# Performance work log

Hardware: AMD Instinct MI355X
Metric: run time of the kernel (lower is better)

The kernel has to match this reference:

```python
import jax, jax.numpy as jnp
import numpy as np

N_T, N_I = 4096, 4096
TEXT_DIM, IMAGE_DIM, HIDDEN_DIM = 1024, 1024, 1024


def setup_inputs() -> dict:
    key = jax.random.key(0)
    ks = jax.random.split(key, 8)
    s_t = 1.0 / np.sqrt(TEXT_DIM)
    s_i = 1.0 / np.sqrt(IMAGE_DIM)
    return {
        "text_features": jax.random.normal(ks[0], (N_T, TEXT_DIM), jnp.float32),
        "image_features": jax.random.normal(ks[1], (N_I, IMAGE_DIM), jnp.float32),
        # nn.Linear params: weight [out, in], bias [out]
        "w_text": jax.random.uniform(ks[2], (HIDDEN_DIM, TEXT_DIM), jnp.float32, -s_t, s_t),
        "b_text": jax.random.uniform(ks[3], (HIDDEN_DIM,), jnp.float32, -s_t, s_t),
        "w_image": jax.random.uniform(ks[4], (HIDDEN_DIM, IMAGE_DIM), jnp.float32, -s_i, s_i),
        "b_image": jax.random.uniform(ks[5], (HIDDEN_DIM,), jnp.float32, -s_i, s_i),
        "scale_TI": jnp.ones((1,), jnp.float32),
        "scale_IT": jnp.ones((1,), jnp.float32),
    }


def reference(text_features, image_features, w_text, b_text, w_image, b_image, scale_TI, scale_IT):
    # linear projections to shared hidden space
    t = text_features @ w_text.T + b_text      # [N_t, H]
    i = image_features @ w_image.T + b_image   # [N_i, H]
    inv_sqrt_h = 1.0 / jnp.sqrt(jnp.asarray(HIDDEN_DIM, t.dtype))
    # text -> image attention: softmax over image axis, scaled post-softmax
    logits_TI = (t @ i.T) * inv_sqrt_h               # [N_t, N_i]
    attn_TI = jax.nn.softmax(logits_TI, axis=-1) * scale_TI
    # image -> text attention
    attn_IT = jax.nn.softmax(logits_TI.T, axis=-1) * scale_IT  # [N_i, N_t]
    text_attention_on_image = attn_TI @ image_features  # [N_t, image_dim]
    image_attention_on_text = attn_IT @ text_features   # [N_i, text_dim]
    return (text_attention_on_image, image_attention_on_text)
```

## Files before the change

### kernel.cpp

```cpp
#include <hip/hip_runtime.h>


typedef __bf16 bf16x8 __attribute__((ext_vector_type(8)));
typedef float f32x4 __attribute__((ext_vector_type(4)));

#define N_T 4096
#define N_I 4096
#define DIM 1024
#define TSS 136

__device__ __forceinline__ unsigned short f2bf(float f) {
    unsigned int u = __float_as_uint(f);
    u += 0x7fffu + ((u >> 16) & 1u);
    return (unsigned short)(u >> 16);
}

__device__ __forceinline__ void async_cp16(const unsigned short* g, unsigned short* l) {
    __builtin_amdgcn_global_load_lds(
        (const __attribute__((address_space(1))) unsigned int*)g,
        (__attribute__((address_space(3))) unsigned int*)l, 16, 0, 0);
}

__device__ __forceinline__ void stage_async(const unsigned short* __restrict__ src,
                                            int ld, int row0, int k0,
                                            unsigned short* lds, int t) {
    int r = t >> 2, c = (t & 3) << 3;
    const unsigned short* g = src + (size_t)(row0 + r) * ld + k0 + c;
    async_cp16(g, lds + r * 32 + c);
    async_cp16(g + (size_t)64 * ld, lds + (64 + r) * 32 + c);
}

__device__ __forceinline__ void mfma_step(const unsigned short* As,
                                          const unsigned short* Bs, f32x4 acc[4][4],
                                          int wrow, int wcol, int lane16, int quad) {
    bf16x8 a[4], b[4];
#pragma unroll
    for (int i = 0; i < 4; ++i) {
        a[i] = *(const bf16x8*)&As[(wrow + i * 16 + lane16) * 32 + quad * 8];
        b[i] = *(const bf16x8*)&Bs[(wcol + i * 16 + lane16) * 32 + quad * 8];
    }
#pragma unroll
    for (int i = 0; i < 4; ++i)
#pragma unroll
        for (int j = 0; j < 4; ++j)
            acc[i][j] = __builtin_amdgcn_mfma_f32_16x16x32_bf16(a[i], b[j], acc[i][j], 0, 0, 0);
}

__device__ __forceinline__ void tile_store(const unsigned short* sm,
                                           unsigned short* __restrict__ g, int ld,
                                           int row0, int col0, int tid) {
    int r = tid >> 1, h = (tid & 1) << 6;
    const unsigned short* src = sm + r * TSS + h;
    unsigned short* dst = g + (size_t)(row0 + r) * ld + col0 + h;
#pragma unroll
    for (int v = 0; v < 8; ++v)
        *(uint4*)(dst + v * 8) = *(const uint4*)(src + v * 8);
}

__global__ void __launch_bounds__(256)
cvt_all(const float* __restrict__ im, const float* __restrict__ tx,
        const float* __restrict__ wt, const float* __restrict__ wi,
        unsigned short* __restrict__ imb, unsigned short* __restrict__ txb,
        unsigned short* __restrict__ imgT, unsigned short* __restrict__ textT,
        unsigned short* __restrict__ wtb, unsigned short* __restrict__ wib,
        float* __restrict__ lTI) {
    int t = threadIdx.x;
    if (blockIdx.z == 2) {
        int lin = blockIdx.y * 64 + blockIdx.x;
        if (lin < 4) {
            *(f32x4*)&lTI[(lin * 256 + t) * 8] = (f32x4){0.f, 0.f, 0.f, 0.f};
            *(f32x4*)&lTI[(lin * 256 + t) * 8 + 4] = (f32x4){0.f, 0.f, 0.f, 0.f};
        }
        size_t i = (size_t)(lin * 256 + t) * 8;
        const float* s;
        unsigned short* d;
        size_t off;
        if (i < 1048576) { s = wt; d = wtb; off = i; }
        else             { s = wi; d = wib; off = i - 1048576; }
        float4 f0 = *(const float4*)(s + off);
        float4 f1 = *(const float4*)(s + off + 4);
        uint4 o;
        o.x = (unsigned int)f2bf(f0.x) | ((unsigned int)f2bf(f0.y) << 16);
        o.y = (unsigned int)f2bf(f0.z) | ((unsigned int)f2bf(f0.w) << 16);
        o.z = (unsigned int)f2bf(f1.x) | ((unsigned int)f2bf(f1.y) << 16);
        o.w = (unsigned int)f2bf(f1.z) | ((unsigned int)f2bf(f1.w) << 16);
        *(uint4*)(d + off) = o;
        return;
    }
    const float* in = blockIdx.z ? tx : im;
    unsigned short* nb = blockIdx.z ? txb : imb;
    unsigned short* tr = blockIdx.z ? textT : imgT;
    __shared__ float tile[64][65];
    int row0 = blockIdx.x * 64, col0 = blockIdx.y * 64;
    int r = t >> 2, c = (t & 3) << 4;
    {
        const float* p = in + (size_t)(row0 + r) * DIM + col0 + c;
        float4 f0 = *(const float4*)(p);
        float4 f1 = *(const float4*)(p + 4);
        float4 f2 = *(const float4*)(p + 8);
        float4 f3 = *(const float4*)(p + 12);
        *(float4*)&tile[r][c] = f0;
        *(float4*)&tile[r][c + 4] = f1;
        *(float4*)&tile[r][c + 8] = f2;
        *(float4*)&tile[r][c + 12] = f3;
        uint4 o0, o1;
        o0.x = (unsigned int)f2bf(f0.x) | ((unsigned int)f2bf(f0.y) << 16);
        o0.y = (unsigned int)f2bf(f0.z) | ((unsigned int)f2bf(f0.w) << 16);
        o0.z = (unsigned int)f2bf(f1.x) | ((unsigned int)f2bf(f1.y) << 16);
        o0.w = (unsigned int)f2bf(f1.z) | ((unsigned int)f2bf(f1.w) << 16);
        o1.x = (unsigned int)f2bf(f2.x) | ((unsigned int)f2bf(f2.y) << 16);
        o1.y = (unsigned int)f2bf(f2.z) | ((unsigned int)f2bf(f2.w) << 16);
        o1.z = (unsigned int)f2bf(f3.x) | ((unsigned int)f2bf(f3.y) << 16);
        o1.w = (unsigned int)f2bf(f3.z) | ((unsigned int)f2bf(f3.w) << 16);
        unsigned short* q = nb + (size_t)(row0 + r) * DIM + col0 + c;
        *(uint4*)q = o0;
        *(uint4*)(q + 8) = o1;
    }
    __syncthreads();
    {
        int cr = r, cc = c;
        unsigned short v[16];
#pragma unroll
        for (int u = 0; u < 16; ++u) v[u] = f2bf(tile[cc + u][cr]);
        unsigned short* q = tr + (size_t)(col0 + cr) * N_T + row0 + cc;
        *(uint4*)q = *(uint4*)&v[0];
        *(uint4*)(q + 8) = *(uint4*)&v[8];
    }
}

__global__ void __launch_bounds__(256, 4)
gemm_proj2(const unsigned short* __restrict__ Atx, const unsigned short* __restrict__ Wtx,
           const float* __restrict__ btx, unsigned short* __restrict__ Ctx,
           const unsigned short* __restrict__ Aim, const unsigned short* __restrict__ Wim,
           const float* __restrict__ bim, unsigned short* __restrict__ Cim) {
    __shared__ unsigned short As[2][128 * 32];
    __shared__ unsigned short Bs[2][128 * 32];
    int z = blockIdx.z;
    const unsigned short* A = z ? Aim : Atx;
    const unsigned short* W = z ? Wim : Wtx;
    const float* bias = z ? bim : btx;
    unsigned short* C = z ? Cim : Ctx;
    int tid = threadIdx.x;
    int m0 = blockIdx.x * 128, n0 = blockIdx.y * 128;
    int lane = tid & 63, wave = tid >> 6;
    int lane16 = lane & 15, quad = lane >> 4;
    int wrow = (wave >> 1) * 64, wcol = (wave & 1) * 64;
    f32x4 acc[4][4];
    {
        f32x4 zz = {0.f, 0.f, 0.f, 0.f};
        for (int i = 0; i < 4; ++i)
            for (int j = 0; j < 4; ++j) acc[i][j] = zz;
    }
    for (int k0 = 0; k0 < DIM; k0 += 64) {
        stage_async(A, DIM, m0, k0, As[0], tid);
        stage_async(W, DIM, n0, k0, Bs[0], tid);
        stage_async(A, DIM, m0, k0 + 32, As[1], tid);
        stage_async(W, DIM, n0, k0 + 32, Bs[1], tid);
        __syncthreads();
        mfma_step(As[0], Bs[0], acc, wrow, wcol, lane16, quad);
        mfma_step(As[1], Bs[1], acc, wrow, wcol, lane16, quad);
        __syncthreads();
    }
#pragma unroll
    for (int j = 0; j < 4; ++j) {
        int col = n0 + wcol + j * 16 + lane16;
        float bv = bias[col];
#pragma unroll
        for (int i = 0; i < 4; ++i) {
            int rowb = m0 + wrow + i * 16 + quad * 4;
#pragma unroll
            for (int r = 0; r < 4; ++r)
                C[(size_t)(rowb + r) * DIM + col] = f2bf(acc[i][j][r] + bv);
        }
    }
}

__global__ void __launch_bounds__(256, 4)
gemm_logits_exp(const unsigned short* __restrict__ Tb,
                const unsigned short* __restrict__ Ib,
                unsigned short* __restrict__ P, unsigned short* __restrict__ PT,
                float* __restrict__ lT, float* __restrict__ lI) {
    __shared__ unsigned short smem[128 * TSS];
    unsigned short* As0 = smem;
    unsigned short* Bs0 = smem + 4096;
    unsigned short* As1 = smem + 8192;
    unsigned short* Bs1 = smem + 12288;
    int tid = threadIdx.x;
    int m0 = blockIdx.x * 128, n0 = blockIdx.y * 128;
    int lane = tid & 63, wave = tid >> 6;
    int lane16 = lane & 15, quad = lane >> 4;
    int wrow = (wave >> 1) * 64, wcol = (wave & 1) * 64;
    f32x4 acc[4][4];
    {
        f32x4 z = {0.f, 0.f, 0.f, 0.f};
        for (int i = 0; i < 4; ++i)
            for (int j = 0; j < 4; ++j) acc[i][j] = z;
    }
    for (int k0 = 0; k0 < DIM; k0 += 64) {
        stage_async(Tb, DIM, m0, k0, As0, tid);
        stage_async(Ib, DIM, n0, k0, Bs0, tid);
        stage_async(Tb, DIM, m0, k0 + 32, As1, tid);
        stage_async(Ib, DIM, n0, k0 + 32, Bs1, tid);
        __syncthreads();
        mfma_step(As0, Bs0, acc, wrow, wcol, lane16, quad);
        mfma_step(As1, Bs1, acc, wrow, wcol, lane16, quad);
        __syncthreads();
    }
#pragma unroll
    for (int i = 0; i < 4; ++i)
#pragma unroll
        for (int j = 0; j < 4; ++j)
#pragma unroll
            for (int r = 0; r < 4; ++r)
                acc[i][j][r] = __expf(acc[i][j][r] * 0.03125f);
#pragma unroll
    for (int i = 0; i < 4; ++i)
#pragma unroll
        for (int r = 0; r < 4; ++r) {
            float s = acc[i][0][r] + acc[i][1][r] + acc[i][2][r] + acc[i][3][r];
            s += __shfl_xor(s, 1); s += __shfl_xor(s, 2);
            s += __shfl_xor(s, 4); s += __shfl_xor(s, 8);
            if (lane16 == 0) atomicAdd(&lT[m0 + wrow + i * 16 + quad * 4 + r], s);
        }
#pragma unroll
    for (int j = 0; j < 4; ++j) {
        float s = 0.f;
#pragma unroll
        for (int i = 0; i < 4; ++i)
#pragma unroll
            for (int r = 0; r < 4; ++r) s += acc[i][j][r];
        s += __shfl_xor(s, 16); s += __shfl_xor(s, 32);
        if (quad == 0) atomicAdd(&lI[n0 + wcol + j * 16 + lane16], s);
    }
    __syncthreads();
#pragma unroll
    for (int i = 0; i < 4; ++i)
#pragma unroll
        for (int j = 0; j < 4; ++j)
#pragma unroll
            for (int r = 0; r < 4; ++r)
                smem[(wrow + i * 16 + quad * 4 + r) * TSS + wcol + j * 16 + lane16] =
                    f2bf(acc[i][j][r]);
    __syncthreads();
    tile_store(smem, P, N_I, m0, n0, tid);
    __syncthreads();
#pragma unroll
    for (int i = 0; i < 4; ++i)
#pragma unroll
        for (int j = 0; j < 4; ++j) {
            unsigned int lo = (unsigned int)f2bf(acc[i][j][0]) |
                              ((unsigned int)f2bf(acc[i][j][1]) << 16);
            unsigned int hi = (unsigned int)f2bf(acc[i][j][2]) |
                              ((unsigned int)f2bf(acc[i][j][3]) << 16);
            uint2 v; v.x = lo; v.y = hi;
            *(uint2*)&smem[(wcol + j * 16 + lane16) * TSS + wrow + i * 16 + quad * 4] = v;
        }
    __syncthreads();
    tile_store(smem, PT, N_T, n0, m0, tid);
}

__global__ void __launch_bounds__(512, 4)
gemm_attn2(const unsigned short* __restrict__ P, const unsigned short* __restrict__ imgT,
           const float* __restrict__ lT, const float* __restrict__ sTI,
           float* __restrict__ out0,
           const unsigned short* __restrict__ PT, const unsigned short* __restrict__ textT,
           const float* __restrict__ lI, const float* __restrict__ sIT,
           float* __restrict__ out1) {
    __shared__ unsigned short As[2][2][128 * 32];
    __shared__ unsigned short Bs[2][2][128 * 32];
    int which = blockIdx.z;
    const unsigned short* A = which ? PT : P;
    const unsigned short* Bt = which ? textT : imgT;
    const float* l = which ? lI : lT;
    const float* sp = which ? sIT : sTI;
    float* out = which ? out1 : out0;

    int tid = threadIdx.x;
    int half = tid >> 8;
    int t = tid & 255;
    int m0 = blockIdx.x * 128, n0 = blockIdx.y * 128;
    int lane = tid & 63;
    int wv = (tid >> 6) & 3;
    int lane16 = lane & 15, quad = lane >> 4;
    int wrow = (wv >> 1) * 64, wcol = (wv & 1) * 64;
    f32x4 acc[4][4];
    {
        f32x4 z = {0.f, 0.f, 0.f, 0.f};
        for (int i = 0; i < 4; ++i)
            for (int j = 0; j < 4; ++j) acc[i][j] = z;
    }

    int kbeg = half * 2048;
    for (int k0 = kbeg; k0 < kbeg + 2048; k0 += 64) {
        stage_async(A, 4096, m0, k0, As[half][0], t);
        stage_async(Bt, 4096, n0, k0, Bs[half][0], t);
        stage_async(A, 4096, m0, k0 + 32, As[half][1], t);
        stage_async(Bt, 4096, n0, k0 + 32, Bs[half][1], t);
        __syncthreads();
        mfma_step(As[half][0], Bs[half][0], acc, wrow, wcol, lane16, quad);
        mfma_step(As[half][1], Bs[half][1], acc, wrow, wcol, lane16, quad);
        __syncthreads();
    }

    float* red = (float*)As;
#pragma unroll
    for (int i = 0; i < 4; ++i) {
        __syncthreads();
        if (half) {
#pragma unroll
            for (int j = 0; j < 4; ++j)
                *(f32x4*)&red[wv * 1024 + lane * 16 + j * 4] = acc[i][j];
        }
        __syncthreads();
        if (!half) {
#pragma unroll
            for (int j = 0; j < 4; ++j)
                acc[i][j] += *(const f32x4*)&red[wv * 1024 + lane * 16 + j * 4];
        }
    }
    if (half) return;

    float sc = sp[0];
#pragma unroll
    for (int i = 0; i < 4; ++i) {
        int rowb = m0 + wrow + i * 16 + quad * 4;
        float fac[4];
#pragma unroll
        for (int r = 0; r < 4; ++r) fac[r] = sc / l[rowb + r];
#pragma unroll
        for (int j = 0; j < 4; ++j) {
            int col = n0 + wcol + j * 16 + lane16;
#pragma unroll
            for (int r = 0; r < 4; ++r)
                out[(size_t)(rowb + r) * DIM + col] = acc[i][j][r] * fac[r];
        }
    }
}

extern "C" void kernel_launch(void* const* d_in, const int* in_sizes, int n_in,
                              void* d_out, int out_size, void* d_ws, size_t ws_size,
                              hipStream_t stream) {
    const float* text = (const float*)d_in[0];
    const float* image = (const float*)d_in[1];
    const float* w_text = (const float*)d_in[2];
    const float* b_text = (const float*)d_in[3];
    const float* w_image = (const float*)d_in[4];
    const float* b_image = (const float*)d_in[5];
    const float* scale_TI = (const float*)d_in[6];
    const float* scale_IT = (const float*)d_in[7];
    float* out0 = (float*)d_out;
    float* out1 = out0 + (size_t)N_T * DIM;

    char* ws = (char*)d_ws;
    unsigned short* text_bf = (unsigned short*)(ws);
    unsigned short* image_bf = (unsigned short*)(ws + (8ull << 20));
    unsigned short* wt_bf = (unsigned short*)(ws + (16ull << 20));
    unsigned short* wi_bf = (unsigned short*)(ws + (18ull << 20));
    unsigned short* P = (unsigned short*)(ws);
    unsigned short* imgT = (unsigned short*)(ws + (32ull << 20));
    unsigned short* textT = (unsigned short*)(ws + (40ull << 20));
    unsigned short* t_bf = (unsigned short*)(ws + (48ull << 20));
    unsigned short* i_bf = (unsigned short*)(ws + (56ull << 20));
    unsigned short* PT = (unsigned short*)(ws + (64ull << 20));
    float* lT = (float*)(ws + (96ull << 20));
    float* lI = (float*)(ws + (96ull << 20) + 16384);

    cvt_all<<<dim3(N_T / 64, DIM / 64, 3), 256, 0, stream>>>(
        image, text, w_text, w_image, image_bf, text_bf, imgT, textT,
        wt_bf, wi_bf, lT);

    gemm_proj2<<<dim3(N_T / 128, DIM / 128, 2), 256, 0, stream>>>(
        text_bf, wt_bf, b_text, t_bf, image_bf, wi_bf, b_image, i_bf);

    gemm_logits_exp<<<dim3(N_T / 128, N_I / 128), 256, 0, stream>>>(t_bf, i_bf, P, PT, lT, lI);

    gemm_attn2<<<dim3(N_T / 128, DIM / 128, 2), 512, 0, stream>>>(
        P, imgT, lT, scale_TI, out0, PT, textT, lI, scale_IT, out1);
}
```

Measured before the change: 267.1 us.

## Halve proj tile width, pre-reduce softmax sums in LDS, split attn epilogue

The projection GEMM now uses 128x64 tiles, doubling the grid to 1024 blocks so the GPU's compute units are better filled. In the logits kernel, row and column exp-sums are first combined across wave pairs in shared memory, which halves the global atomicAdds. In the split-K attention kernel, the reduction now runs in two steps with fewer barriers, and both halves share the scaling and output stores. The cost is less data reuse per block in the projection GEMM and a small amount of extra LDS and synchronisation in the logits kernel.

```diff
diff --git a/kernel.cpp b/kernel.cpp
--- a/kernel.cpp
+++ b/kernel.cpp
@@ -30,6 +30,13 @@
     async_cp16(g + (size_t)64 * ld, lds + (64 + r) * 32 + c);
 }
 
+__device__ __forceinline__ void stage_async64(const unsigned short* __restrict__ src,
+                                              int ld, int row0, int k0,
+                                              unsigned short* lds, int t) {
+    int r = t >> 2, c = (t & 3) << 3;
+    async_cp16(src + (size_t)(row0 + r) * ld + k0 + c, lds + r * 32 + c);
+}
+
 __device__ __forceinline__ void mfma_step(const unsigned short* As,
                                           const unsigned short* Bs, f32x4 acc[4][4],
                                           int wrow, int wcol, int lane16, int quad) {
@@ -43,6 +50,23 @@
     for (int i = 0; i < 4; ++i)
 #pragma unroll
         for (int j = 0; j < 4; ++j)
+            acc[i][j] = __builtin_amdgcn_mfma_f32_16x16x32_bf16(a[i], b[j], acc[i][j], 0, 0, 0);
+}
+
+__device__ __forceinline__ void mfma_step42(const unsigned short* As,
+                                            const unsigned short* Bs, f32x4 acc[4][2],
+                                            int wrow, int wcol, int lane16, int quad) {
+    bf16x8 a[4], b[2];
+#pragma unroll
+    for (int i = 0; i < 4; ++i)
+        a[i] = *(const bf16x8*)&As[(wrow + i * 16 + lane16) * 32 + quad * 8];
+#pragma unroll
+    for (int j = 0; j < 2; ++j)
+        b[j] = *(const bf16x8*)&Bs[(wcol + j * 16 + lane16) * 32 + quad * 8];
+#pragma unroll
+    for (int i = 0; i < 4; ++i)
+#pragma unroll
+        for (int j = 0; j < 2; ++j)
             acc[i][j] = __builtin_amdgcn_mfma_f32_16x16x32_bf16(a[i], b[j], acc[i][j], 0, 0, 0);
 }
 
@@ -118,11 +142,10 @@
     }
     __syncthreads();
     {
-        int cr = r, cc = c;
         unsigned short v[16];
 #pragma unroll
-        for (int u = 0; u < 16; ++u) v[u] = f2bf(tile[cc + u][cr]);
-        unsigned short* q = tr + (size_t)(col0 + cr) * N_T + row0 + cc;
+        for (int u = 0; u < 16; ++u) v[u] = f2bf(tile[c + u][r]);
+        unsigned short* q = tr + (size_t)(col0 + r) * N_T + row0 + c;
         *(uint4*)q = *(uint4*)&v[0];
         *(uint4*)(q + 8) = *(uint4*)&v[8];
     }
@@ -134,35 +157,35 @@
            const unsigned short* __restrict__ Aim, const unsigned short* __restrict__ Wim,
            const float* __restrict__ bim, unsigned short* __restrict__ Cim) {
     __shared__ unsigned short As[2][128 * 32];
-    __shared__ unsigned short Bs[2][128 * 32];
+    __shared__ unsigned short Bs[2][64 * 32];
     int z = blockIdx.z;
     const unsigned short* A = z ? Aim : Atx;
     const unsigned short* W = z ? Wim : Wtx;
     const float* bias = z ? bim : btx;
     unsigned short* C = z ? Cim : Ctx;
     int tid = threadIdx.x;
-    int m0 = blockIdx.x * 128, n0 = blockIdx.y * 128;
+    int m0 = blockIdx.x * 128, n0 = blockIdx.y * 64;
     int lane = tid & 63, wave = tid >> 6;
     int lane16 = lane & 15, quad = lane >> 4;
-    int wrow = (wave >> 1) * 64, wcol = (wave & 1) * 64;
-    f32x4 acc[4][4];
+    int wrow = (wave >> 1) * 64, wcol = (wave & 1) * 32;
+    f32x4 acc[4][2];
     {
         f32x4 zz = {0.f, 0.f, 0.f, 0.f};
         for (int i = 0; i < 4; ++i)
-            for (int j = 0; j < 4; ++j) acc[i][j] = zz;
+            for (int j = 0; j < 2; ++j) acc[i][j] = zz;
     }
     for (int k0 = 0; k0 < DIM; k0 += 64) {
         stage_async(A, DIM, m0, k0, As[0], tid);
-        stage_async(W, DIM, n0, k0, Bs[0], tid);
+        stage_async64(W, DIM, n0, k0, Bs[0], tid);
         stage_async(A, DIM, m0, k0 + 32, As[1], tid);
-        stage_async(W, DIM, n0, k0 + 32, Bs[1], tid);
-        __syncthreads();
-        mfma_step(As[0], Bs[0], acc, wrow, wcol, lane16, quad);
-        mfma_step(As[1], Bs[1], acc, wrow, wcol, lane16, quad);
-        __syncthreads();
-    }
-#pragma unroll
-    for (int j = 0; j < 4; ++j) {
+        stage_async64(W, DIM, n0, k0 + 32, Bs[1], tid);
+        __syncthreads();
+        mfma_step42(As[0], Bs[0], acc, wrow, wcol, lane16, quad);
+        mfma_step42(As[1], Bs[1], acc, wrow, wcol, lane16, quad);
+        __syncthreads();
+    }
+#pragma unroll
+    for (int j = 0; j < 2; ++j) {
         int col = n0 + wcol + j * 16 + lane16;
         float bv = bias[col];
 #pragma unroll
@@ -185,6 +208,8 @@
     unsigned short* Bs0 = smem + 4096;
     unsigned short* As1 = smem + 8192;
     unsigned short* Bs1 = smem + 12288;
+    float* lred = (float*)(smem + 16384);
+    float* cred = lred + 128;
     int tid = threadIdx.x;
     int m0 = blockIdx.x * 128, n0 = blockIdx.y * 128;
     int lane = tid & 63, wave = tid >> 6;
@@ -213,6 +238,7 @@
 #pragma unroll
             for (int r = 0; r < 4; ++r)
                 acc[i][j][r] = __expf(acc[i][j][r] * 0.03125f);
+    float rs[4][4];
 #pragma unroll
     for (int i = 0; i < 4; ++i)
 #pragma unroll
@@ -220,8 +246,9 @@
             float s = acc[i][0][r] + acc[i][1][r] + acc[i][2][r] + acc[i][3][r];
             s += __shfl_xor(s, 1); s += __shfl_xor(s, 2);
             s += __shfl_xor(s, 4); s += __shfl_xor(s, 8);
-            if (lane16 == 0) atomicAdd(&lT[m0 + wrow + i * 16 + quad * 4 + r], s);
-        }
+            rs[i][r] = s;
+        }
+    float cs[4];
 #pragma unroll
     for (int j = 0; j < 4; ++j) {
         float s = 0.f;
@@ -230,7 +257,38 @@
 #pragma unroll
             for (int r = 0; r < 4; ++r) s += acc[i][j][r];
         s += __shfl_xor(s, 16); s += __shfl_xor(s, 32);
-        if (quad == 0) atomicAdd(&lI[n0 + wcol + j * 16 + lane16], s);
+        cs[j] = s;
+    }
+    if (wave & 1) {
+        if (lane16 == 0)
+#pragma unroll
+            for (int i = 0; i < 4; ++i)
+#pragma unroll
+                for (int r = 0; r < 4; ++r)
+                    lred[wrow + i * 16 + quad * 4 + r] = rs[i][r];
+    }
+    if (wave >> 1) {
+        if (quad == 0)
+#pragma unroll
+            for (int j = 0; j < 4; ++j)
+                cred[wcol + j * 16 + lane16] = cs[j];
+    }
+    __syncthreads();
+    if (!(wave & 1) && lane16 == 0) {
+#pragma unroll
+        for (int i = 0; i < 4; ++i)
+#pragma unroll
+            for (int r = 0; r < 4; ++r) {
+                int row = wrow + i * 16 + quad * 4 + r;
+                atomicAdd(&lT[m0 + row], rs[i][r] + lred[row]);
+            }
+    }
+    if (!(wave >> 1) && quad == 0) {
+#pragma unroll
+        for (int j = 0; j < 4; ++j) {
+            int col = wcol + j * 16 + lane16;
+            atomicAdd(&lI[n0 + col], cs[j] + cred[col]);
+        }
     }
     __syncthreads();
 #pragma unroll
@@ -303,27 +361,41 @@
     }
 
     float* red = (float*)As;
-#pragma unroll
-    for (int i = 0; i < 4; ++i) {
-        __syncthreads();
-        if (half) {
+    if (half) {
+#pragma unroll
+        for (int i = 0; i < 2; ++i)
 #pragma unroll
             for (int j = 0; j < 4; ++j)
-                *(f32x4*)&red[wv * 1024 + lane * 16 + j * 4] = acc[i][j];
-        }
-        __syncthreads();
-        if (!half) {
+                *(f32x4*)&red[(wv * 2 + i) * 1024 + lane * 16 + j * 4] = acc[i][j];
+    }
+    __syncthreads();
+    if (!half) {
+#pragma unroll
+        for (int i = 0; i < 2; ++i)
 #pragma unroll
             for (int j = 0; j < 4; ++j)
-                acc[i][j] += *(const f32x4*)&red[wv * 1024 + lane * 16 + j * 4];
-        }
-    }
-    if (half) return;
+                acc[i][j] += *(const f32x4*)&red[(wv * 2 + i) * 1024 + lane * 16 + j * 4];
+#pragma unroll
+        for (int i = 2; i < 4; ++i)
+#pragma unroll
+            for (int j = 0; j < 4; ++j)
+                *(f32x4*)&red[(wv * 2 + i - 2) * 1024 + lane * 16 + j * 4] = acc[i][j];
+    }
+    __syncthreads();
+    if (half) {
+#pragma unroll
+        for (int i = 2; i < 4; ++i)
+#pragma unroll
+            for (int j = 0; j < 4; ++j)
+                acc[i][j] += *(const f32x4*)&red[(wv * 2 + i - 2) * 1024 + lane * 16 + j * 4];
+    }
 
     float sc = sp[0];
-#pragma unroll
-    for (int i = 0; i < 4; ++i) {
-        int rowb = m0 + wrow + i * 16 + quad * 4;
+    int ibeg = half ? 2 : 0;
+#pragma unroll
+    for (int i = 0; i < 2; ++i) {
+        int ii = ibeg + i;
+        int rowb = m0 + wrow + ii * 16 + quad * 4;
         float fac[4];
 #pragma unroll
         for (int r = 0; r < 4; ++r) fac[r] = sc / l[rowb + r];
@@ -332,7 +404,7 @@
             int col = n0 + wcol + j * 16 + lane16;
 #pragma unroll
             for (int r = 0; r < 4; ++r)
-                out[(size_t)(rowb + r) * DIM + col] = acc[i][j][r] * fac[r];
+                out[(size_t)(rowb + r) * DIM + col] = acc[ii][j][r] * fac[r];
         }
     }
 }
@@ -369,7 +441,7 @@
         image, text, w_text, w_image, image_bf, text_bf, imgT, textT,
         wt_bf, wi_bf, lT);
 
-    gemm_proj2<<<dim3(N_T / 128, DIM / 128, 2), 256, 0, stream>>>(
+    gemm_proj2<<<dim3(N_T / 128, DIM / 64, 2), 256, 0, stream>>>(
         text_bf, wt_bf, b_text, t_bf, image_bf, wi_bf, b_image, i_bf);
 
     gemm_logits_exp<<<dim3(N_T / 128, N_I / 128), 256, 0, stream>>>(t_bf, i_bf, P, PT, lT, lI);
```

Result: slower. 546.5 us (+104.6%).
